# Kernel optimization log

Hardware: AMD Instinct MI355X
Metric: run time of the kernel (lower is better)

The kernel has to match this reference:

```python
import jax, jax.numpy as jnp
import numpy as np

H = 768; NH = 12; DH = H // NH; E = 2; R = 128; B = 32; S = 512
SCALE = 1.0 / np.sqrt(DH)


def _mha_core(q, k, v, mask):
    # q,k,v: [B,S,H] projected; mask: [B,S] (1 = keep)
    b, s, _ = q.shape
    qh = q.reshape(b, s, NH, DH)
    kh = k.reshape(b, s, NH, DH)
    vh = v.reshape(b, s, NH, DH)
    scores = jnp.einsum('bqhd,bkhd->bhqk', qh, kh) * SCALE
    scores = scores + (1.0 - mask)[:, None, None, :] * (-10000.0)
    probs = jax.nn.softmax(scores, axis=-1)
    return jnp.einsum('bhqk,bkhd->bqhd', probs, vh).reshape(b, s, H)


def _forward(x, switch_w, switch_b, c_wq, c_bq, c_wk, c_bk, c_wv, c_bv, c_wo, c_bo,
             e_wq, e_bq, e_aq, e_gq, e_wk, e_bk, e_ak, e_gk, e_wv, e_bv, e_av, e_gv,
             e_wo, e_bo, attention_mask):
    # --- switch routing (per-sample, mean-pooled over sequence) ---
    logits = x.mean(axis=1) @ switch_w + switch_b          # [B,E]
    route_prob = jax.nn.softmax(logits, axis=-1)
    route_prob_max = route_prob.max(axis=-1)               # [B]
    routes = jnp.argmax(route_prob, axis=-1)               # [B]
    onehot = jax.nn.one_hot(routes, E, dtype=x.dtype)      # [B,E] dense equivalent of gather/scatter dispatch

    # --- LoRA attention experts (vmapped over experts) ---
    def lora_expert(wq, bq, aq, gq, wk, bk, ak, gk, wv, bv, av, gv, wo, bo):
        q = x @ wq + bq + (x @ aq) @ gq
        k = x @ wk + bk + (x @ ak) @ gk
        v = x @ wv + bv + (x @ av) @ gv
        return _mha_core(q, k, v, attention_mask) @ wo + bo   # [B,S,H]

    expert_out = jax.vmap(lora_expert)(e_wq, e_bq, e_aq, e_gq, e_wk, e_bk, e_ak, e_gk,
                                       e_wv, e_bv, e_av, e_gv, e_wo, e_bo)  # [E,B,S,H]
    routed = jnp.einsum('ebsh,be->bsh', expert_out, onehot)

    # scaling factor = p_max / stop_grad(p_max) (forward identity, grad path to router)
    scaling = (route_prob_max / jax.lax.stop_gradient(route_prob_max))[:, None, None]
    routed = routed * scaling

    # --- common (shared) attention expert ---
    q = x @ c_wq + c_bq
    k = x @ c_wk + c_bk
    v = x @ c_wv + c_bv
    common = _mha_core(q, k, v, attention_mask) @ c_wo + c_bo
    return routed + common


def setup_inputs() -> dict:
    key = jax.random.key(0)
    ks = jax.random.split(key, 32)
    std = 0.02
    def w(i, shape):
        return jax.random.normal(ks[i], shape, jnp.float32) * std
    z = lambda shape: jnp.zeros(shape, jnp.float32)
    return {
        'x': jax.random.normal(ks[0], (B, S, H), jnp.float32),
        'switch_w': w(1, (H, E)), 'switch_b': z((E,)),
        'c_wq': w(2, (H, H)), 'c_bq': z((H,)),
        'c_wk': w(3, (H, H)), 'c_bk': z((H,)),
        'c_wv': w(4, (H, H)), 'c_bv': z((H,)),
        'c_wo': w(5, (H, H)), 'c_bo': z((H,)),
        'e_wq': w(6, (E, H, H)), 'e_bq': z((E, H)),
        'e_aq': w(7, (E, H, R)), 'e_gq': w(8, (E, R, H)),
        'e_wk': w(9, (E, H, H)), 'e_bk': z((E, H)),
        'e_ak': w(10, (E, H, R)), 'e_gk': w(11, (E, R, H)),
        'e_wv': w(12, (E, H, H)), 'e_bv': z((E, H)),
        'e_av': w(13, (E, H, R)), 'e_gv': w(14, (E, R, H)),
        'e_wo': w(15, (E, H, H)), 'e_bo': z((E, H)),
        'attention_mask': jnp.ones((B, S), jnp.float32),
    }


def reference(x, switch_w, switch_b, c_wq, c_bq, c_wk, c_bk, c_wv, c_bv, c_wo, c_bo,
              e_wq, e_bq, e_aq, e_gq, e_wk, e_bk, e_ak, e_gk, e_wv, e_bv, e_av, e_gv,
              e_wo, e_bo, attention_mask):
    return _forward(x, switch_w, switch_b, c_wq, c_bq, c_wk, c_bk, c_wv, c_bv, c_wo, c_bo,
                    e_wq, e_bq, e_aq, e_gq, e_wk, e_bk, e_ak, e_gk, e_wv, e_bv, e_av, e_gv,
                    e_wo, e_bo, attention_mask)
```

## Files before the change

kernel.cpp:

```cpp
#include <hip/hip_runtime.h>
#include <hip/hip_bf16.h>

#define DEVINL __device__ __forceinline__

typedef __bf16 bf16x8 __attribute__((ext_vector_type(8)));
typedef float f32x4 __attribute__((ext_vector_type(4)));
typedef unsigned short u16x8 __attribute__((ext_vector_type(8)));
typedef unsigned short u16x4 __attribute__((ext_vector_type(4)));

DEVINL unsigned short f2bf(float f) {
  __hip_bfloat16 h = __float2bfloat16(f);
  return __builtin_bit_cast(unsigned short, h);
}

DEVINL float bf2f(unsigned short u) {
  return __builtin_bit_cast(float, ((unsigned)u) << 16);
}

DEVINL f32x4 mfma16(bf16x8 a, bf16x8 b, f32x4 c) {
  return __builtin_amdgcn_mfma_f32_16x16x32_bf16(a, b, c, 0, 0, 0);
}

DEVINL void gload_lds16(const void* g, void* l) {
  __builtin_amdgcn_global_load_lds(
      (const __attribute__((address_space(1))) unsigned int*)g,
      (__attribute__((address_space(3))) unsigned int*)l, 16, 0, 0);
}

__global__ __launch_bounds__(256) void k_cvt(const float* __restrict__ x,
                                             u16x8* __restrict__ xb) {
  int i = blockIdx.x * 256 + threadIdx.x;
  const float* p = x + (size_t)i * 8;
  float4 a = *(const float4*)p;
  float4 b = *(const float4*)(p + 4);
  u16x8 o;
  o[0] = f2bf(a.x); o[1] = f2bf(a.y); o[2] = f2bf(a.z); o[3] = f2bf(a.w);
  o[4] = f2bf(b.x); o[5] = f2bf(b.y); o[6] = f2bf(b.z); o[7] = f2bf(b.w);
  xb[i] = o;
}

__global__ __launch_bounds__(256) void k_xsum(const float* __restrict__ x,
                                              float* __restrict__ xsum) {
  int b = blockIdx.x, sc = blockIdx.z;
  int h = blockIdx.y * 256 + threadIdx.x;
  float s = 0.f;
  const float* p = x + ((size_t)(b * 512 + sc * 128)) * 768 + h;
  for (int i = 0; i < 128; ++i) s += p[(size_t)i * 768];
  xsum[(sc * 32 + b) * 768 + h] = s;
}

__global__ __launch_bounds__(256) void k_route(const float* __restrict__ xsum,
                                               const float* __restrict__ sw,
                                               const float* __restrict__ sb,
                                               int* __restrict__ route) {
  int b = blockIdx.x, t = threadIdx.x;
  float l0 = 0.f, l1 = 0.f;
  for (int h = t; h < 768; h += 256) {
    float xm = (xsum[(0 * 32 + b) * 768 + h] + xsum[(1 * 32 + b) * 768 + h] +
                xsum[(2 * 32 + b) * 768 + h] + xsum[(3 * 32 + b) * 768 + h]) *
               (1.f / 512.f);
    l0 += xm * sw[h * 2 + 0];
    l1 += xm * sw[h * 2 + 1];
  }
#pragma unroll
  for (int off = 32; off; off >>= 1) {
    l0 += __shfl_down(l0, off);
    l1 += __shfl_down(l1, off);
  }
  __shared__ float s0[4], s1[4];
  int w = t >> 6;
  if ((t & 63) == 0) { s0[w] = l0; s1[w] = l1; }
  __syncthreads();
  if (t == 0) {
    float a0 = sb[0] + s0[0] + s0[1] + s0[2] + s0[3];
    float a1 = sb[1] + s1[0] + s1[1] + s1[2] + s1[3];
    route[b] = (a1 > a0) ? 1 : 0;
  }
}

__global__ __launch_bounds__(256) void k_wt(const float* __restrict__ cwq, const float* __restrict__ cwk,
                                            const float* __restrict__ cwv, const float* __restrict__ cwo,
                                            const float* __restrict__ ewo,
                                            const float* __restrict__ ewq, const float* __restrict__ ewk,
                                            const float* __restrict__ ewv,
                                            unsigned short* __restrict__ wtc,
                                            unsigned short* __restrict__ wtewo,
                                            unsigned short* __restrict__ wtexp) {
  __shared__ float t[32][33];
  int z = blockIdx.z;
  const float* src;
  unsigned short* dst;
  if (z < 4) {
    src = (z == 0) ? cwq : (z == 1) ? cwk : (z == 2) ? cwv : cwo;
    dst = wtc + (size_t)z * 589824;
  } else if (z < 6) {
    src = ewo + (size_t)(z - 4) * 589824;
    dst = wtewo + (size_t)(z - 4) * 589824;
  } else {
    int mat = (z - 6) >> 1, e = (z - 6) & 1;
    src = ((mat == 0) ? ewq : (mat == 1) ? ewk : ewv) + (size_t)e * 589824;
    dst = wtexp + (size_t)(mat * 2 + e) * 589824;
  }
  int k0 = blockIdx.x * 32, n0 = blockIdx.y * 32;
  int tid = threadIdx.x;
#pragma unroll
  for (int i = 0; i < 4; ++i) {
    int lin = tid + 256 * i; int kk = lin >> 5, nn = lin & 31;
    t[kk][nn] = src[(size_t)(k0 + kk) * 768 + n0 + nn];
  }
  __syncthreads();
#pragma unroll
  for (int i = 0; i < 4; ++i) {
    int lin = tid + 256 * i; int nn = lin >> 5, kk = lin & 31;
    dst[(size_t)(n0 + nn) * 768 + k0 + kk] = f2bf(t[kk][nn]);
  }
}

__global__ __launch_bounds__(256) void k_acvt(const float* __restrict__ eaq, const float* __restrict__ eak,
                                              const float* __restrict__ eav,
                                              unsigned short* __restrict__ abt) {
  int z = blockIdx.z;
  int mat = z >> 1, e = z & 1;
  const float* src = ((mat == 0) ? eaq : (mat == 1) ? eak : eav) + (size_t)e * 98304;
  unsigned short* dst = abt + (size_t)z * 98304;
  int i = blockIdx.x * 256 + threadIdx.x;
  const float* p = src + (size_t)i * 8;
  float4 a = *(const float4*)p;
  float4 b = *(const float4*)(p + 4);
  u16x8 o;
  o[0] = f2bf(a.x); o[1] = f2bf(a.y); o[2] = f2bf(a.z); o[3] = f2bf(a.w);
  o[4] = f2bf(b.x); o[5] = f2bf(b.y); o[6] = f2bf(b.z); o[7] = f2bf(b.w);
  *(u16x8*)(dst + (size_t)i * 8) = o;
}

__global__ __launch_bounds__(256) void k_gtr(const float* __restrict__ egq, const float* __restrict__ egk,
                                             const float* __restrict__ egv,
                                             unsigned short* __restrict__ gtb) {
  __shared__ float t[32][33];
  int z = blockIdx.z;
  int mat = z >> 1, e = z & 1;
  const float* src = ((mat == 0) ? egq : (mat == 1) ? egk : egv) + (size_t)e * 98304;
  unsigned short* dst = gtb + (size_t)z * 98304;
  int n0 = blockIdx.x * 32, r0 = blockIdx.y * 32;
  int tid = threadIdx.x;
#pragma unroll
  for (int i = 0; i < 4; ++i) {
    int lin = tid + 256 * i; int rr = lin >> 5, nn = lin & 31;
    t[rr][nn] = src[(size_t)(r0 + rr) * 768 + n0 + nn];
  }
  __syncthreads();
#pragma unroll
  for (int i = 0; i < 4; ++i) {
    int lin = tid + 256 * i; int nn = lin >> 5, rr = lin & 31;
    dst[(size_t)(n0 + nn) * 128 + r0 + rr] = f2bf(t[rr][nn]);
  }
}

__global__ __launch_bounds__(256) void k_mergemm(const unsigned short* __restrict__ gtb,
                                                 const unsigned short* __restrict__ abt,
                                                 const unsigned short* __restrict__ wtexp,
                                                 unsigned short* __restrict__ wte) {
  const int z = blockIdx.z;
  const int m0 = blockIdx.x * 128, n0 = blockIdx.y * 128;
  const unsigned short* Am = gtb + (size_t)z * 98304;
  const unsigned short* Bm = abt + (size_t)z * 98304;
  const unsigned short* Wt = wtexp + (size_t)z * 589824;
  unsigned short* dst = wte + (size_t)z * 589824;
  __shared__ __align__(16) unsigned short As[128 * 32];
  __shared__ __align__(16) unsigned short Bs[128 * 32];
  const int tid = threadIdx.x, w = tid >> 6, lane = tid & 63, g = lane >> 4, l15 = lane & 15;
  const int wr = (w >> 1) * 64, wc = (w & 1) * 64;
  f32x4 acc[4][4] = {};
  for (int k0 = 0; k0 < 128; k0 += 32) {
#pragma unroll
    for (int c = 0; c < 2; ++c) {
      int o = (w * 2 + c) * 1024 + lane * 16;
      int row = o >> 6, chunk = (o >> 4) & 3;
      gload_lds16(Am + (size_t)(m0 + row) * 128 + k0 + (chunk << 3),
                  (char*)As + (w * 2 + c) * 1024);
      gload_lds16(Bm + (size_t)(n0 + row) * 128 + k0 + (chunk << 3),
                  (char*)Bs + (w * 2 + c) * 1024);
    }
    __syncthreads();
    bf16x8 af[4], bfr[4];
#pragma unroll
    for (int mi = 0; mi < 4; ++mi) {
      int row = wr + mi * 16 + l15;
      af[mi] = *(const bf16x8*)((const char*)As + row * 64 + (g << 4));
    }
#pragma unroll
    for (int ni = 0; ni < 4; ++ni) {
      int row = wc + ni * 16 + l15;
      bfr[ni] = *(const bf16x8*)((const char*)Bs + row * 64 + (g << 4));
    }
#pragma unroll
    for (int mi = 0; mi < 4; ++mi)
#pragma unroll
      for (int ni = 0; ni < 4; ++ni)
        acc[mi][ni] = mfma16(af[mi], bfr[ni], acc[mi][ni]);
    __syncthreads();
  }
#pragma unroll
  for (int ni = 0; ni < 4; ++ni) {
    int col = n0 + wc + ni * 16 + l15;
#pragma unroll
    for (int mi = 0; mi < 4; ++mi) {
#pragma unroll
      for (int r = 0; r < 4; ++r) {
        int row = m0 + wr + mi * 16 + 4 * g + r;
        size_t idx = (size_t)row * 768 + col;
        dst[idx] = f2bf(acc[mi][ni][r] + bf2f(Wt[idx]));
      }
    }
  }
}

template <int MH, int KK, bool LOADB>
DEVINL void qphase(const unsigned short* As, const unsigned short* Bs,
                   bf16x8 (&bfr)[4], f32x4 (&acc)[8][4],
                   int wr, int wc, int g, int l15) {
  if (LOADB) {
#pragma unroll
    for (int nj = 0; nj < 4; ++nj) {
      int row = wc + nj * 16 + l15;
      bfr[nj] = *(const bf16x8*)((const char*)Bs + row * 128 + (((KK * 4 + g) ^ (row & 7)) << 4));
    }
  }
  bf16x8 af[4];
#pragma unroll
  for (int mi = 0; mi < 4; ++mi) {
    int row = wr + MH * 64 + mi * 16 + l15;
    af[mi] = *(const bf16x8*)((const char*)As + row * 128 + (((KK * 4 + g) ^ (row & 7)) << 4));
  }
  __builtin_amdgcn_s_setprio(1);
#pragma unroll
  for (int mi = 0; mi < 4; ++mi)
#pragma unroll
    for (int nj = 0; nj < 4; ++nj)
      acc[MH * 4 + mi][nj] = mfma16(af[mi], bfr[nj], acc[MH * 4 + mi][nj]);
  __builtin_amdgcn_s_setprio(0);
}

__global__ __launch_bounds__(512, 2) void k_gemm_qkv(
    const unsigned short* __restrict__ xb, const unsigned short* __restrict__ wtc,
    const unsigned short* __restrict__ wte,
    const float* __restrict__ cbq, const float* __restrict__ cbk, const float* __restrict__ cbv,
    const float* __restrict__ ebq, const float* __restrict__ ebk, const float* __restrict__ ebv,
    const int* __restrict__ route,
    unsigned short* __restrict__ qC, unsigned short* __restrict__ kC, unsigned short* __restrict__ vC,
    unsigned short* __restrict__ qE, unsigned short* __restrict__ kE, unsigned short* __restrict__ vE,
    int base_expert) {
  extern __shared__ __align__(16) unsigned short smem[];
  const int m0 = blockIdx.x * 256, n0 = blockIdx.y * 256;
  const int mat = blockIdx.z % 3;
  const int expert = base_expert + blockIdx.z / 3;
  const int b = m0 >> 9;
  const unsigned short* wt;
  const float* bias;
  if (!expert) {
    wt = wtc + (size_t)mat * 589824;
    bias = (mat == 0) ? cbq : (mat == 1) ? cbk : cbv;
  } else {
    int e = route[b];
    wt = wte + (size_t)(mat * 2 + e) * 589824;
    bias = ((mat == 0) ? ebq : (mat == 1) ? ebk : ebv) + e * 768;
  }
  unsigned short* outq = expert ? qE : qC;
  unsigned short* outk = expert ? kE : kC;
  unsigned short* vt   = expert ? vE : vC;
  const int tid = threadIdx.x, w = tid >> 6, lane = tid & 63, g = lane >> 4, l15 = lane & 15;
  const int wr = (w >> 2) * 128, wc = (w & 3) * 64;
  const int srow = lane >> 3, sslot = lane & 7;
  f32x4 acc[8][4] = {};

  auto stage_half = [&](int buf, int t, int h) {
    const unsigned short* src = (h < 2) ? xb : wt;
    int rowbase = (h < 2) ? (m0 + h * 128) : (n0 + (h - 2) * 128);
    unsigned short* lb = smem + buf * 32768 + ((h < 2) ? (h * 8192) : (16384 + (h - 2) * 8192));
    int k0 = t * 64;
#pragma unroll
    for (int c = 0; c < 2; ++c) {
      int rl = (w * 2 + c) * 8 + srow;
      int gc = (sslot ^ (rl & 7)) << 3;
      gload_lds16(src + (size_t)(rowbase + rl) * 768 + k0 + gc,
                  (char*)lb + (w * 2 + c) * 1024);
    }
  };

#pragma unroll
  for (int h = 0; h < 4; ++h) stage_half(0, 0, h);
  int cur = 0;
  for (int t = 0; t < 12; ++t) {
    const int nxt = cur ^ 1;
    const int tn = (t + 1 < 12) ? (t + 1) : 0;
    const unsigned short* As = smem + cur * 32768;
    const unsigned short* Bs = smem + cur * 32768 + 16384;
    bf16x8 bfr[4];
    stage_half(nxt, tn, 0);
    stage_half(nxt, tn, 2);
    asm volatile("s_waitcnt vmcnt(4)" ::: "memory");
    asm volatile("s_barrier" ::: "memory");
    qphase<0, 0, true>(As, Bs, bfr, acc, wr, wc, g, l15);
    stage_half(nxt, tn, 1);
    stage_half(nxt, tn, 3);
    asm volatile("s_barrier" ::: "memory");
    qphase<1, 0, false>(As, Bs, bfr, acc, wr, wc, g, l15);
    asm volatile("s_barrier" ::: "memory");
    qphase<0, 1, true>(As, Bs, bfr, acc, wr, wc, g, l15);
    asm volatile("s_barrier" ::: "memory");
    qphase<1, 1, false>(As, Bs, bfr, acc, wr, wc, g, l15);
    asm volatile("s_barrier" ::: "memory");
    cur = nxt;
  }
  __syncthreads();

  if (mat != 2) {
    unsigned short* pw = smem + w * 8192;
#pragma unroll
    for (int nj = 0; nj < 4; ++nj) {
      float bv = bias[n0 + wc + nj * 16 + l15];
#pragma unroll
      for (int fr = 0; fr < 8; ++fr)
#pragma unroll
        for (int r = 0; r < 4; ++r) {
          int lr = fr * 16 + 4 * g + r;
          int lc = nj * 16 + l15;
          pw[lr * 64 + (((lc >> 3) ^ (lr & 7)) << 3) + (lc & 7)] =
              f2bf(acc[fr][nj][r] + bv);
        }
    }
    unsigned short* dst = (mat == 0) ? outq : outk;
#pragma unroll
    for (int i = 0; i < 16; ++i) {
      int ci = i * 64 + lane;
      int row = ci >> 3;
      int c8 = ci & 7;
      u16x8 v = *(const u16x8*)(pw + row * 64 + ((c8 ^ (row & 7)) << 3));
      *(u16x8*)(dst + (size_t)(m0 + wr + row) * 768 + n0 + wc + c8 * 8) = v;
    }
  } else {
    unsigned short* Ts2 = smem;
#pragma unroll
    for (int p = 0; p < 2; ++p) {
      if (((w & 3) >> 1) == p) {
#pragma unroll
        for (int nj = 0; nj < 4; ++nj) {
          int ccl = ((w & 3) & 1) * 64 + nj * 16 + l15;
          float bv = bias[n0 + p * 128 + ccl];
#pragma unroll
          for (int fr = 0; fr < 8; ++fr)
#pragma unroll
            for (int r = 0; r < 4; ++r) {
              int row = wr + fr * 16 + 4 * g + r;
              Ts2[ccl * 264 + row] = f2bf(acc[fr][nj][r] + bv);
            }
        }
      }
      __syncthreads();
#pragma unroll
      for (int i = 0; i < 8; ++i) {
        int ci = tid + 512 * i, cc = ci >> 5, j = ci & 31;
        u16x8 v = *(const u16x8*)(Ts2 + cc * 264 + j * 8);
        int colg = n0 + p * 128 + cc;
        int head = colg >> 6, dh = colg & 63;
        *(u16x8*)(vt + ((size_t)((b * 12 + head) * 64 + dh)) * 512 + (m0 & 511) + j * 8) = v;
      }
      __syncthreads();
    }
  }
}

__global__ __launch_bounds__(512) void k_attn(
    const unsigned short* __restrict__ Q0, const unsigned short* __restrict__ K0,
    const unsigned short* __restrict__ V0, unsigned short* __restrict__ ctx0,
    const unsigned short* __restrict__ Q1, const unsigned short* __restrict__ K1,
    const unsigned short* __restrict__ V1, unsigned short* __restrict__ ctx1,
    const float* __restrict__ mask) {
  const int qh = blockIdx.x, h = blockIdx.y;
  const int b = blockIdx.z & 31, path = blockIdx.z >> 5;
  const unsigned short* Q = path ? Q1 : Q0;
  const unsigned short* K = path ? K1 : K0;
  const unsigned short* Vt = path ? V1 : V0;
  unsigned short* ctx = path ? ctx1 : ctx0;
  const int tid = threadIdx.x, w = tid >> 6, lane = tid & 63, g = lane >> 4, l15 = lane & 15;
  const int qbase = b * 512 + qh * 256 + w * 32;
  bf16x8 qf[2][2];
#pragma unroll
  for (int qs = 0; qs < 2; ++qs) {
    const unsigned short* qp = Q + (size_t)(qbase + qs * 16 + l15) * 768 + h * 64;
    qf[qs][0] = *(const bf16x8*)(qp + g * 8);
    qf[qs][1] = *(const bf16x8*)(qp + 32 + g * 8);
  }
  __shared__ __align__(16) unsigned short Ks[64 * 64];
  __shared__ __align__(16) unsigned short Vs[64 * 64];
  __shared__ __align__(16) unsigned short Pl[8 * 16 * 64];
  __shared__ float mk2[64];
  float lsum[2] = {0.f, 0.f};
  f32x4 acc[2][4] = {};
  const unsigned short* Kb = K + (size_t)(b * 512) * 768 + h * 64;
  const unsigned short* Vb = Vt + (size_t)((b * 12 + h) * 64) * 512;
  unsigned short* pws = Pl + w * 1024;
  const int srow = w * 8 + (lane >> 3);
  const int schunk = lane & 7;
  const int ssw = (schunk ^ (srow & 7)) << 3;
  const float C = 0.125f * 1.44269504f;
  for (int kt = 0; kt < 8; ++kt) {
    const int kv0 = kt * 64;
    gload_lds16(Kb + (size_t)(kv0 + srow) * 768 + ssw, (char*)Ks + w * 1024);
    gload_lds16(Vb + (size_t)srow * 512 + kv0 + ssw, (char*)Vs + w * 1024);
    if (tid < 64) mk2[tid] = (1.f - mask[b * 512 + kv0 + tid]) * (-14426.9504f);
    __syncthreads();
#pragma unroll
    for (int qs = 0; qs < 2; ++qs) {
      f32x4 sf[4];
#pragma unroll
      for (int mb = 0; mb < 4; ++mb) {
        int row = mb * 16 + l15;
        bf16x8 ka  = *(const bf16x8*)(Ks + row * 64 + ((g ^ (row & 7)) << 3));
        bf16x8 kb2 = *(const bf16x8*)(Ks + row * 64 + (((g + 4) ^ (row & 7)) << 3));
        f32x4 z = {0.f, 0.f, 0.f, 0.f};
        z = mfma16(ka, qf[qs][0], z);
        z = mfma16(kb2, qf[qs][1], z);
        sf[mb] = z;
      }
      float p[16];
      float psum = 0.f;
#pragma unroll
      for (int mb = 0; mb < 4; ++mb)
#pragma unroll
        for (int r = 0; r < 4; ++r) {
          float e2 = exp2f(fmaf(sf[mb][r], C, mk2[mb * 16 + g * 4 + r]));
          p[mb * 4 + r] = e2;
          psum += e2;
        }
      lsum[qs] += psum;
#pragma unroll
      for (int mb = 0; mb < 4; ++mb)
#pragma unroll
        for (int hh = 0; hh < 2; ++hh) {
          unsigned val = (unsigned)f2bf(p[mb * 4 + 2 * hh]) |
                         ((unsigned)f2bf(p[mb * 4 + 2 * hh + 1]) << 16);
          int off = mb * 16 + 4 * g + 2 * hh;
          int cw = (off >> 3) ^ (l15 & 7);
          *(unsigned*)(pws + l15 * 64 + (cw << 3) + (off & 7)) = val;
        }
#pragma unroll
      for (int ks = 0; ks < 2; ++ks) {
        bf16x8 pf = *(const bf16x8*)(pws + l15 * 64 + (((4 * ks + g) ^ (l15 & 7)) << 3));
#pragma unroll
        for (int d = 0; d < 4; ++d) {
          int row = d * 16 + l15;
          bf16x8 vf = *(const bf16x8*)(Vs + row * 64 + (((g + 4 * ks) ^ (row & 7)) << 3));
          acc[qs][d] = mfma16(vf, pf, acc[qs][d]);
        }
      }
    }
    __syncthreads();
  }
#pragma unroll
  for (int qs = 0; qs < 2; ++qs) {
    float t = lsum[qs];
    t += __shfl_xor(t, 16);
    t += __shfl_xor(t, 32);
    float inv = 1.f / t;
    unsigned short* op = ctx + (size_t)(qbase + qs * 16 + l15) * 768 + h * 64;
#pragma unroll
    for (int d = 0; d < 4; ++d) {
      u16x4 o4;
#pragma unroll
      for (int r = 0; r < 4; ++r) o4[r] = f2bf(acc[qs][d][r] * inv);
      *(u16x4*)(op + d * 16 + 4 * g) = o4;
    }
  }
}

__global__ __launch_bounds__(512, 2) void k_gemm_out(
    const unsigned short* __restrict__ ctxc, const unsigned short* __restrict__ ctxe,
    const unsigned short* __restrict__ woc, const unsigned short* __restrict__ woe,
    const float* __restrict__ cbo, const float* __restrict__ ebo,
    const int* __restrict__ route, float* __restrict__ out) {
  extern __shared__ __align__(16) unsigned short smem[];
  const int m0 = blockIdx.x * 256, n0 = blockIdx.y * 256;
  const int b = m0 >> 9;
  const int e = route[b];
  const int tid = threadIdx.x, w = tid >> 6, lane = tid & 63, g = lane >> 4, l15 = lane & 15;
  const int wr = (w >> 2) * 128, wc = (w & 3) * 64;
  const int srow = lane >> 3, sslot = lane & 7;
  f32x4 acc[8][4] = {};

  auto stage_half = [&](int buf, int t, int h) {
    const unsigned short* src =
        (h < 2) ? ((t < 12) ? ctxc : ctxe)
                : ((t < 12) ? woc : (woe + (size_t)e * 589824));
    int rowbase = (h < 2) ? (m0 + h * 128) : (n0 + (h - 2) * 128);
    unsigned short* lb = smem + buf * 32768 + ((h < 2) ? (h * 8192) : (16384 + (h - 2) * 8192));
    int k0 = (t % 12) * 64;
#pragma unroll
    for (int c = 0; c < 2; ++c) {
      int rl = (w * 2 + c) * 8 + srow;
      int gc = (sslot ^ (rl & 7)) << 3;
      gload_lds16(src + (size_t)(rowbase + rl) * 768 + k0 + gc,
                  (char*)lb + (w * 2 + c) * 1024);
    }
  };

#pragma unroll
  for (int h = 0; h < 4; ++h) stage_half(0, 0, h);
  int cur = 0;
  for (int t = 0; t < 24; ++t) {
    const int nxt = cur ^ 1;
    const int tn = (t + 1 < 24) ? (t + 1) : 0;
    const unsigned short* As = smem + cur * 32768;
    const unsigned short* Bs = smem + cur * 32768 + 16384;
    bf16x8 bfr[4];
    stage_half(nxt, tn, 0);
    stage_half(nxt, tn, 2);
    asm volatile("s_waitcnt vmcnt(4)" ::: "memory");
    asm volatile("s_barrier" ::: "memory");
    qphase<0, 0, true>(As, Bs, bfr, acc, wr, wc, g, l15);
    stage_half(nxt, tn, 1);
    stage_half(nxt, tn, 3);
    asm volatile("s_barrier" ::: "memory");
    qphase<1, 0, false>(As, Bs, bfr, acc, wr, wc, g, l15);
    asm volatile("s_barrier" ::: "memory");
    qphase<0, 1, true>(As, Bs, bfr, acc, wr, wc, g, l15);
    asm volatile("s_barrier" ::: "memory");
    qphase<1, 1, false>(As, Bs, bfr, acc, wr, wc, g, l15);
    asm volatile("s_barrier" ::: "memory");
    cur = nxt;
  }
  __syncthreads();

  float* fs = (float*)smem;
#pragma unroll
  for (int p = 0; p < 4; ++p) {
    if ((w >> 2) == (p >> 1)) {
#pragma unroll
      for (int nj = 0; nj < 4; ++nj) {
        int lc = wc + nj * 16 + l15;
        int col = n0 + lc;
        float bsum = cbo[col] + ebo[e * 768 + col];
#pragma unroll
        for (int fi = 0; fi < 4; ++fi) {
          int fr = (p & 1) * 4 + fi;
#pragma unroll
          for (int r = 0; r < 4; ++r) {
            int lr = fi * 16 + 4 * g + r;
            fs[lr * 256 + (((lc >> 2) ^ (lr & 7)) << 2) + (lc & 3)] =
                acc[fr][nj][r] + bsum;
          }
        }
      }
    }
    __syncthreads();
#pragma unroll
    for (int j = 0; j < 8; ++j) {
      int ci = j * 512 + tid;
      int row = ci >> 6, sl = ci & 63;
      f32x4 v = *(const f32x4*)(fs + row * 256 + ((sl ^ (row & 7)) << 2));
      *(f32x4*)(out + (size_t)(m0 + p * 64 + row) * 768 + n0 + sl * 4) = v;
    }
    __syncthreads();
  }
}

extern "C" void kernel_launch(void* const* d_in, const int* in_sizes, int n_in,
                              void* d_out, int out_size, void* d_ws, size_t ws_size,
                              hipStream_t stream) {
  const float* x    = (const float*)d_in[0];
  const float* sw   = (const float*)d_in[1];
  const float* sb   = (const float*)d_in[2];
  const float* cwq  = (const float*)d_in[3];
  const float* cbq  = (const float*)d_in[4];
  const float* cwk  = (const float*)d_in[5];
  const float* cbk  = (const float*)d_in[6];
  const float* cwv  = (const float*)d_in[7];
  const float* cbv  = (const float*)d_in[8];
  const float* cwo  = (const float*)d_in[9];
  const float* cbo  = (const float*)d_in[10];
  const float* ewq  = (const float*)d_in[11];
  const float* ebq  = (const float*)d_in[12];
  const float* eaq  = (const float*)d_in[13];
  const float* egq  = (const float*)d_in[14];
  const float* ewk  = (const float*)d_in[15];
  const float* ebk  = (const float*)d_in[16];
  const float* eak  = (const float*)d_in[17];
  const float* egk  = (const float*)d_in[18];
  const float* ewv  = (const float*)d_in[19];
  const float* ebv  = (const float*)d_in[20];
  const float* eav  = (const float*)d_in[21];
  const float* egv  = (const float*)d_in[22];
  const float* ewo  = (const float*)d_in[23];
  const float* ebo  = (const float*)d_in[24];
  const float* amask = (const float*)d_in[25];
  (void)in_sizes; (void)n_in; (void)out_size;

  (void)hipFuncSetAttribute(reinterpret_cast<const void*>(k_gemm_qkv),
                            hipFuncAttributeMaxDynamicSharedMemorySize, 131072);
  (void)hipFuncSetAttribute(reinterpret_cast<const void*>(k_gemm_out),
                            hipFuncAttributeMaxDynamicSharedMemorySize, 131072);

  char* ws = (char*)d_ws;
  const size_t SZ = 25165824;
  const size_t MERGED_NEED = 8 * SZ + 4718592 + 7077888 + 2359296 + 393216 + 256;
  const bool merged = (ws_size >= MERGED_NEED);

  unsigned short *xb, *qbC, *kC, *vC, *qbE, *kE, *vE, *ctxc, *ctxe;
  char* wbase;
  if (merged) {
    xb   = (unsigned short*)(ws);
    qbC  = (unsigned short*)(ws + SZ);
    kC   = (unsigned short*)(ws + 2 * SZ);
    vC   = (unsigned short*)(ws + 3 * SZ);
    qbE  = (unsigned short*)(ws + 4 * SZ);
    kE   = (unsigned short*)(ws + 5 * SZ);
    vE   = (unsigned short*)(ws + 6 * SZ);
    ctxc = (unsigned short*)(ws + 7 * SZ);
    ctxe = (unsigned short*)(ws);
    wbase = ws + 8 * SZ;
  } else {
    xb   = (unsigned short*)(ws);
    qbC  = qbE = (unsigned short*)(ws + SZ);
    kC   = kE  = (unsigned short*)(ws + 2 * SZ);
    vC   = vE  = (unsigned short*)(ws + 3 * SZ);
    ctxc = (unsigned short*)(ws + 4 * SZ);
    ctxe = (unsigned short*)(ws);
    wbase = ws + 5 * SZ;
  }
  unsigned short* wtc   = (unsigned short*)(wbase);
  unsigned short* wte   = (unsigned short*)(wbase + 4718592);
  unsigned short* wtewo = (unsigned short*)(wbase + 4718592 + 7077888);
  float* xsum           = (float*)(wbase + 4718592 + 7077888 + 2359296);
  int* route            = (int*)(wbase + 4718592 + 7077888 + 2359296 + 393216);
  unsigned short* abt   = (unsigned short*)(ws + SZ);
  unsigned short* gtb   = (unsigned short*)(ws + SZ + 1179648);
  unsigned short* wtexp = (unsigned short*)(ws + SZ + 2359296);

  k_cvt<<<6144, 256, 0, stream>>>(x, (u16x8*)xb);
  k_xsum<<<dim3(32, 3, 4), 256, 0, stream>>>(x, xsum);
  k_route<<<32, 256, 0, stream>>>(xsum, sw, sb, route);
  k_wt<<<dim3(24, 24, 12), 256, 0, stream>>>(cwq, cwk, cwv, cwo, ewo, ewq, ewk, ewv,
                                             wtc, wtewo, wtexp);
  k_acvt<<<dim3(48, 1, 6), 256, 0, stream>>>(eaq, eak, eav, abt);
  k_gtr<<<dim3(24, 4, 6), 256, 0, stream>>>(egq, egk, egv, gtb);
  k_mergemm<<<dim3(6, 6, 6), 256, 0, stream>>>(gtb, abt, wtexp, wte);

  if (merged) {
    k_gemm_qkv<<<dim3(64, 3, 6), 512, 131072, stream>>>(
        xb, wtc, wte, cbq, cbk, cbv, ebq, ebk, ebv, route,
        qbC, kC, vC, qbE, kE, vE, 0);
    k_attn<<<dim3(2, 12, 64), 512, 0, stream>>>(qbC, kC, vC, ctxc,
                                                qbE, kE, vE, ctxe, amask);
  } else {
    k_gemm_qkv<<<dim3(64, 3, 3), 512, 131072, stream>>>(
        xb, wtc, wte, cbq, cbk, cbv, ebq, ebk, ebv, route,
        qbC, kC, vC, qbC, kC, vC, 0);
    k_attn<<<dim3(2, 12, 32), 512, 0, stream>>>(qbC, kC, vC, ctxc,
                                                qbC, kC, vC, ctxc, amask);
    k_gemm_qkv<<<dim3(64, 3, 3), 512, 131072, stream>>>(
        xb, wtc, wte, cbq, cbk, cbv, ebq, ebk, ebv, route,
        qbC, kC, vC, qbC, kC, vC, 1);
    k_attn<<<dim3(2, 12, 32), 512, 0, stream>>>(qbC, kC, vC, ctxe,
                                                qbC, kC, vC, ctxe, amask);
  }
  k_gemm_out<<<dim3(64, 3), 512, 131072, stream>>>(ctxc, ctxe, wtc + 3 * 589824, wtewo,
                                                   cbo, ebo, route, (float*)d_out);
}
```

Baseline: 349.4 us.

## Double-buffer K/V tiles in attention kernel with async prefetch

The attention kernel now keeps two LDS buffers for K and V. It issues the global_load_lds for the next key tile before computing on the current one, and uses manual vmcnt waits and s_barrier in place of full __syncthreads. The mask bias for all 512 keys is also computed once into shared memory up front, not per tile. This is meant to hide global-load latency behind the MFMA and softmax work. In exchange it doubles K/V LDS use, which may lower occupancy, loads one redundant tile on the last iteration, and depends on correct hand-written waitcnt ordering.

Measured after the change: 353.6 us. No clear change (+1.2%).

```diff
diff --git a/kernel.cpp b/kernel.cpp
--- a/kernel.cpp
+++ b/kernel.cpp
@@ -391,10 +391,10 @@
     qf[qs][0] = *(const bf16x8*)(qp + g * 8);
     qf[qs][1] = *(const bf16x8*)(qp + 32 + g * 8);
   }
-  __shared__ __align__(16) unsigned short Ks[64 * 64];
-  __shared__ __align__(16) unsigned short Vs[64 * 64];
+  __shared__ __align__(16) unsigned short Ks[2][64 * 64];
+  __shared__ __align__(16) unsigned short Vs[2][64 * 64];
   __shared__ __align__(16) unsigned short Pl[8 * 16 * 64];
-  __shared__ float mk2[64];
+  __shared__ float mk2[512];
   float lsum[2] = {0.f, 0.f};
   f32x4 acc[2][4] = {};
   const unsigned short* Kb = K + (size_t)(b * 512) * 768 + h * 64;
@@ -404,20 +404,33 @@
   const int schunk = lane & 7;
   const int ssw = (schunk ^ (srow & 7)) << 3;
   const float C = 0.125f * 1.44269504f;
+
+  auto stage = [&](int buf, int kt) {
+    const int kv0 = kt * 64;
+    gload_lds16(Kb + (size_t)(kv0 + srow) * 768 + ssw, (char*)Ks[buf] + w * 1024);
+    gload_lds16(Vb + (size_t)srow * 512 + kv0 + ssw, (char*)Vs[buf] + w * 1024);
+  };
+
+  stage(0, 0);
+  mk2[tid] = (1.f - mask[b * 512 + tid]) * (-14426.9504f);
+  __syncthreads();
+
+  int cur = 0;
   for (int kt = 0; kt < 8; ++kt) {
     const int kv0 = kt * 64;
-    gload_lds16(Kb + (size_t)(kv0 + srow) * 768 + ssw, (char*)Ks + w * 1024);
-    gload_lds16(Vb + (size_t)srow * 512 + kv0 + ssw, (char*)Vs + w * 1024);
-    if (tid < 64) mk2[tid] = (1.f - mask[b * 512 + kv0 + tid]) * (-14426.9504f);
-    __syncthreads();
+    stage(cur ^ 1, (kt + 1 < 8) ? (kt + 1) : 0);
+    asm volatile("s_waitcnt vmcnt(2)" ::: "memory");
+    asm volatile("s_barrier" ::: "memory");
+    const unsigned short* Kc = Ks[cur];
+    const unsigned short* Vc = Vs[cur];
 #pragma unroll
     for (int qs = 0; qs < 2; ++qs) {
       f32x4 sf[4];
 #pragma unroll
       for (int mb = 0; mb < 4; ++mb) {
         int row = mb * 16 + l15;
-        bf16x8 ka  = *(const bf16x8*)(Ks + row * 64 + ((g ^ (row & 7)) << 3));
-        bf16x8 kb2 = *(const bf16x8*)(Ks + row * 64 + (((g + 4) ^ (row & 7)) << 3));
+        bf16x8 ka  = *(const bf16x8*)(Kc + row * 64 + ((g ^ (row & 7)) << 3));
+        bf16x8 kb2 = *(const bf16x8*)(Kc + row * 64 + (((g + 4) ^ (row & 7)) << 3));
         f32x4 z = {0.f, 0.f, 0.f, 0.f};
         z = mfma16(ka, qf[qs][0], z);
         z = mfma16(kb2, qf[qs][1], z);
@@ -429,7 +442,7 @@
       for (int mb = 0; mb < 4; ++mb)
 #pragma unroll
         for (int r = 0; r < 4; ++r) {
-          float e2 = exp2f(fmaf(sf[mb][r], C, mk2[mb * 16 + g * 4 + r]));
+          float e2 = exp2f(fmaf(sf[mb][r], C, mk2[kv0 + mb * 16 + g * 4 + r]));
           p[mb * 4 + r] = e2;
           psum += e2;
         }
@@ -450,12 +463,13 @@
 #pragma unroll
         for (int d = 0; d < 4; ++d) {
           int row = d * 16 + l15;
-          bf16x8 vf = *(const bf16x8*)(Vs + row * 64 + (((g + 4 * ks) ^ (row & 7)) << 3));
+          bf16x8 vf = *(const bf16x8*)(Vc + row * 64 + (((g + 4 * ks) ^ (row & 7)) << 3));
           acc[qs][d] = mfma16(vf, pf, acc[qs][d]);
         }
       }
     }
-    __syncthreads();
+    asm volatile("s_barrier" ::: "memory");
+    cur ^= 1;
   }
 #pragma unroll
   for (int qs = 0; qs < 2; ++qs) {
```
